# Performance work log

Hardware: AMD Instinct MI355X
Metric: run time of the kernel (lower is better)

Reference implementation:

```python
import jax, jax.numpy as jnp
import numpy as np

N = 8192      # nodes (= hidden_channels / heads)
E = 262144    # edges (avg degree 32)
IN = 256      # in_channels
H = 8         # heads
C = 32        # out_channels per head
NEG_SLOPE = 0.2


def setup_inputs() -> dict:
    key = jax.random.key(0)
    ks = jax.random.split(key, 8)
    x = jax.random.normal(ks[0], (N, IN), jnp.float32)
    edge_index = jax.random.randint(ks[1], (2, E), 0, N, dtype=jnp.int32)
    lin_w = jax.random.normal(ks[2], (H * C, IN), jnp.float32) * (1.0 / np.sqrt(IN))
    att_src = jax.random.normal(ks[3], (H, C), jnp.float32) * 0.1
    att_dst = jax.random.normal(ks[4], (H, C), jnp.float32) * 0.1
    bias = jax.random.normal(ks[5], (H * C,), jnp.float32) * 0.01
    out_w = jax.random.normal(ks[6], (C, N * H * C), jnp.float32) * (1.0 / np.sqrt(N * H * C))
    out_b = jax.random.normal(ks[7], (C,), jnp.float32) * 0.01
    return {"x": x, "edge_index": edge_index, "lin_w": lin_w, "att_src": att_src,
            "att_dst": att_dst, "bias": bias, "out_w": out_w, "out_b": out_b}


def reference(x, edge_index, lin_w, att_src, att_dst, bias, out_w, out_b):
    n = x.shape[0]
    # PyG GATConv default: add self loops
    loop = jnp.arange(n, dtype=edge_index.dtype)
    src = jnp.concatenate([edge_index[0], loop])  # message sources j
    dst = jnp.concatenate([edge_index[1], loop])  # message targets i
    # per-head linear projection: [n, H, C]
    xh = (x @ lin_w.T).reshape(n, H, C)
    a_src = jnp.einsum('nhc,hc->nh', xh, att_src)  # [n, H]
    a_dst = jnp.einsum('nhc,hc->nh', xh, att_dst)  # [n, H]
    # edge attention logits + segment softmax over incoming edges of each dst
    e = jax.nn.leaky_relu(a_src[src] + a_dst[dst], negative_slope=NEG_SLOPE)  # [E', H]
    m = jax.ops.segment_max(e, dst, num_segments=n)        # [n, H]
    ex = jnp.exp(e - m[dst])
    denom = jax.ops.segment_sum(ex, dst, num_segments=n)   # [n, H]
    alpha = ex / denom[dst]                                 # [E', H]
    # weighted scatter-add aggregation
    agg = jax.ops.segment_sum(alpha[:, :, None] * xh[src], dst, num_segments=n)  # [n, H, C]
    out = agg.reshape(n, H * C) + bias
    # flatten all nodes, dense output layer, softmax
    y = out.reshape(-1) @ out_w.T + out_b  # [C]
    return jax.nn.softmax(y)
```

## Files before the change

### kernel.cpp

```cpp
#include <hip/hip_runtime.h>


namespace {
constexpr int  kN    = 8192;
constexpr int  kE    = 262144;
constexpr int  kTotE = kE + kN;
constexpr long kK    = 2097152;
constexpr int  kYB   = 256;
}

typedef float vfloat4 __attribute__((ext_vector_type(4)));

static __device__ __forceinline__ ushort f2bf(float f) {
  unsigned u = __float_as_uint(f);
  return (ushort)((u + 0x7FFFu + ((u >> 16) & 1u)) >> 16);
}
static __device__ __forceinline__ float bf2f(ushort b) {
  return __uint_as_float(((unsigned)b) << 16);
}

__global__ __launch_bounds__(256) void gemm_att_hist(const float* __restrict__ x,
                                                     const float* __restrict__ lw,
                                                     const float* __restrict__ att_s,
                                                     const float* __restrict__ att_d,
                                                     const int* __restrict__ ei,
                                                     ushort* __restrict__ xh_bf,
                                                     float* __restrict__ a_src,
                                                     float* __restrict__ a_dst,
                                                     int* __restrict__ cnt) {
  __shared__ float As[16][68];
  __shared__ float Bs[16][68];
  const int t  = threadIdx.x;
  const int tx = t & 15, ty = t >> 4;
  const int rowBase = blockIdx.x * 64;
  const int colBase = blockIdx.y * 64;
  const int lr = t >> 2;
  const int lk = (t & 3) * 4;

  {
    const int bid = blockIdx.y * 128 + blockIdx.x;
    const int gid = bid * 512 + t;
    atomicAdd(&cnt[ei[kE + gid]], 1);
    atomicAdd(&cnt[ei[kE + gid + 256]], 1);
  }

  float acc[4][4] = {};
  for (int kc = 0; kc < 256; kc += 16) {
    float4 av = *(const float4*)(x  + (long)(rowBase + lr) * 256 + kc + lk);
    float4 bv = *(const float4*)(lw + (long)(colBase + lr) * 256 + kc + lk);
    __syncthreads();
    As[lk + 0][lr] = av.x; As[lk + 1][lr] = av.y; As[lk + 2][lr] = av.z; As[lk + 3][lr] = av.w;
    Bs[lk + 0][lr] = bv.x; Bs[lk + 1][lr] = bv.y; Bs[lk + 2][lr] = bv.z; Bs[lk + 3][lr] = bv.w;
    __syncthreads();
#pragma unroll
    for (int k = 0; k < 16; k++) {
      float4 a4 = *(const float4*)(&As[k][ty * 4]);
      float4 b4 = *(const float4*)(&Bs[k][tx * 4]);
      float aa[4] = {a4.x, a4.y, a4.z, a4.w};
      float bb[4] = {b4.x, b4.y, b4.z, b4.w};
#pragma unroll
      for (int i = 0; i < 4; i++)
#pragma unroll
        for (int j = 0; j < 4; j++) acc[i][j] += aa[i] * bb[j];
    }
  }

#pragma unroll
  for (int i = 0; i < 4; i++) {
    const long row = rowBase + ty * 4 + i;
    ushort4 ob = make_ushort4(f2bf(acc[i][0]), f2bf(acc[i][1]),
                              f2bf(acc[i][2]), f2bf(acc[i][3]));
    *(ushort4*)(xh_bf + row * 256 + colBase + tx * 4) = ob;
  }

  float4 as4 = *(const float4*)(att_s + colBase + tx * 4);
  float4 ad4 = *(const float4*)(att_d + colBase + tx * 4);
#pragma unroll
  for (int i = 0; i < 4; i++) {
    float s = acc[i][0] * as4.x + acc[i][1] * as4.y + acc[i][2] * as4.z + acc[i][3] * as4.w;
    float d = acc[i][0] * ad4.x + acc[i][1] * ad4.y + acc[i][2] * ad4.z + acc[i][3] * ad4.w;
#pragma unroll
    for (int off = 4; off; off >>= 1) {
      s += __shfl_down(s, off, 8);
      d += __shfl_down(d, off, 8);
    }
    if ((tx & 7) == 0) {
      const int row  = rowBase + ty * 4 + i;
      const int head = blockIdx.y * 2 + (tx >> 3);
      a_src[row * 8 + head] = s;
      a_dst[row * 8 + head] = d;
    }
  }
}

__global__ __launch_bounds__(1024) void scan_cnt(const int* __restrict__ cnt,
                                                 int* __restrict__ rowptr,
                                                 int* __restrict__ wpos) {
  __shared__ int wsum[16];
  const int t = threadIdx.x, lane = t & 63, w = t >> 6;
  int v[8]; int sum = 0;
#pragma unroll
  for (int q = 0; q < 8; q++) { v[q] = cnt[t * 8 + q] + 1; sum += v[q]; }
  int sc = sum;
#pragma unroll
  for (int off = 1; off < 64; off <<= 1) {
    int n = __shfl_up(sc, off, 64);
    if (lane >= off) sc += n;
  }
  if (lane == 63) wsum[w] = sc;
  __syncthreads();
  if (t < 16) {
    int ws = wsum[t];
#pragma unroll
    for (int off = 1; off < 16; off <<= 1) {
      int n = __shfl_up(ws, off, 16);
      if ((t & 15) >= off) ws += n;
    }
    wsum[t] = ws;
  }
  __syncthreads();
  int excl = (w ? wsum[w - 1] : 0) + sc - sum;
#pragma unroll
  for (int q = 0; q < 8; q++) {
    rowptr[t * 8 + q] = excl;
    wpos[t * 8 + q]   = excl;
    excl += v[q];
  }
  if (t == 1023) rowptr[kN] = excl;
}

__global__ __launch_bounds__(256) void scatter_csr(const int* __restrict__ ei,
                                                   const float* __restrict__ a_src,
                                                   const float* __restrict__ a_dst,
                                                   int* __restrict__ wpos,
                                                   int* __restrict__ csr,
                                                   float* __restrict__ w8) {
  int idx = blockIdx.x * 256 + threadIdx.x;
  if (idx >= kTotE) return;
  int s, d;
  if (idx < kE) { s = ei[idx]; d = ei[kE + idx]; }
  else          { s = idx - kE; d = s; }
  int pos = atomicAdd(&wpos[d], 1);
  csr[pos] = s;
  float4 s0 = *(const float4*)(a_src + s * 8);
  float4 s1 = *(const float4*)(a_src + s * 8 + 4);
  float4 d0 = *(const float4*)(a_dst + d * 8);
  float4 d1 = *(const float4*)(a_dst + d * 8 + 4);
  float e[8] = {s0.x + d0.x, s0.y + d0.y, s0.z + d0.z, s0.w + d0.w,
                s1.x + d1.x, s1.y + d1.y, s1.z + d1.z, s1.w + d1.w};
  float w[8];
#pragma unroll
  for (int h = 0; h < 8; h++) {
    float ee = (e[h] > 0.f) ? e[h] : 0.2f * e[h];
    w[h] = __expf(ee);
  }
  float4* wp = (float4*)(w8 + (long)pos * 8);
  wp[0] = make_float4(w[0], w[1], w[2], w[3]);
  wp[1] = make_float4(w[4], w[5], w[6], w[7]);
}

__global__ __launch_bounds__(256) void agg_dot(const ushort* __restrict__ xb,
                                               const float* __restrict__ w8,
                                               const int* __restrict__ rowptr,
                                               const int* __restrict__ csr,
                                               const float* __restrict__ bias,
                                               const float* __restrict__ w,
                                               float* __restrict__ ypart) {
  const int i = blockIdx.x, t = threadIdx.x, h = t >> 5;
  const int lane = t & 63, wid = t >> 6;

  const long wbase = (long)i * 256 + lane * 4;
  vfloat4 wv[8];
#pragma unroll
  for (int cc = 0; cc < 8; cc++) {
    const int c = cc * 4 + wid;
    wv[cc] = __builtin_nontemporal_load((const vfloat4*)(w + (long)c * kK + wbase));
  }

  const int beg = rowptr[i], end = rowptr[i + 1];
  float acc = 0.f, den = 0.f;
  int j = beg;
  for (; j + 8 <= end; j += 8) {
    int   s[8]; float ww[8]; float f[8];
#pragma unroll
    for (int q = 0; q < 8; q++) s[q] = csr[j + q];
#pragma unroll
    for (int q = 0; q < 8; q++) ww[q] = w8[(long)(j + q) * 8 + h];
#pragma unroll
    for (int q = 0; q < 8; q++) f[q] = bf2f(xb[(long)s[q] * 256 + t]);
#pragma unroll
    for (int q = 0; q < 8; q++) { den += ww[q]; acc += ww[q] * f[q]; }
  }
  for (; j < end; j++) {
    int s0 = csr[j];
    float w0 = w8[(long)j * 8 + h];
    den += w0;
    acc += w0 * bf2f(xb[(long)s0 * 256 + t]);
  }

  __shared__ float ofs[256];
  __shared__ float yb[32];
  ofs[t] = acc / den + bias[t];
  __syncthreads();
  float4 f4 = *(const float4*)(ofs + lane * 4);
#pragma unroll
  for (int cc = 0; cc < 8; cc++) {
    float p = wv[cc].x * f4.x + wv[cc].y * f4.y + wv[cc].z * f4.z + wv[cc].w * f4.w;
    p += __shfl_down(p, 32, 64);
    p += __shfl_down(p, 16, 64);
    p += __shfl_down(p, 8, 64);
    p += __shfl_down(p, 4, 64);
    p += __shfl_down(p, 2, 64);
    p += __shfl_down(p, 1, 64);
    if (lane == 0) yb[cc * 4 + wid] = p;
  }
  __syncthreads();
  if (t < 32) atomicAdd(&ypart[(i & (kYB - 1)) * 32 + t], yb[t]);
}

__global__ __launch_bounds__(1024) void finalize(const float* __restrict__ ypart,
                                                 const float* __restrict__ ob,
                                                 float* __restrict__ out) {
  __shared__ float s[32][33];
  const int t = threadIdx.x;
  const int c = t & 31, r = t >> 5;
  float sum = 0.f;
  for (int q = r; q < kYB; q += 32) sum += ypart[q * 32 + c];
  s[c][r] = sum;
  __syncthreads();
  if (t < 32) {
    float y = ob[t];
#pragma unroll
    for (int r2 = 0; r2 < 32; r2++) y += s[t][r2];
    float m = y;
#pragma unroll
    for (int off = 16; off; off >>= 1) m = fmaxf(m, __shfl_xor(m, off, 32));
    float e = __expf(y - m);
    float d = e;
#pragma unroll
    for (int off = 16; off; off >>= 1) d += __shfl_xor(d, off, 32);
    out[t] = e / d;
  }
}

extern "C" void kernel_launch(void* const* d_in, const int* in_sizes, int n_in,
                              void* d_out, int out_size, void* d_ws, size_t ws_size,
                              hipStream_t stream) {
  (void)in_sizes; (void)n_in; (void)out_size; (void)ws_size;
  const float* x     = (const float*)d_in[0];
  const int*   ei    = (const int*)  d_in[1];
  const float* lin_w = (const float*)d_in[2];
  const float* att_s = (const float*)d_in[3];
  const float* att_d = (const float*)d_in[4];
  const float* bias  = (const float*)d_in[5];
  const float* out_w = (const float*)d_in[6];
  const float* out_b = (const float*)d_in[7];
  float* out = (float*)d_out;

  float*  a_src    = (float*)d_ws;
  float*  a_dst    = a_src + kN * 8;
  float*  w8       = a_dst + kN * 8;
  ushort* xh_bf    = (ushort*)(w8 + (long)kTotE * 8);
  int*    cnt      = (int*)(xh_bf + kK);
  float*  ypart    = (float*)(cnt + kN);
  int*    rowptr   = (int*)(ypart + kYB * 32);
  int*    wpos     = rowptr + (kN + 1);
  int*    csr      = wpos + kN;

  (void)hipMemsetAsync(cnt, 0, kN * sizeof(int) + kYB * 32 * sizeof(float), stream);
  gemm_att_hist<<<dim3(128, 4), 256, 0, stream>>>(x, lin_w, att_s, att_d, ei,
                                                  xh_bf, a_src, a_dst, cnt);
  scan_cnt   <<<1, 1024, 0, stream>>>(cnt, rowptr, wpos);
  scatter_csr<<<(kTotE + 255) / 256, 256, 0, stream>>>(ei, a_src, a_dst, wpos, csr, w8);
  agg_dot    <<<kN, 256, 0, stream>>>(xh_bf, w8, rowptr, csr, bias, out_w, ypart);
  finalize   <<<1, 1024, 0, stream>>>(ypart, out_b, out);
}
```

Before: 427.0 us.

## Compute edge attention weights inside aggregation instead of materializing w8

Edge weights (leaky-relu plus exp of a_src+a_dst) are no longer computed in the CSR scatter kernel and written to an E'x8 buffer. The aggregation kernel now recomputes them from a_src gathered per source and a_dst per destination. This removes the write and reread of roughly 8.7 MB of per-edge weights and the scatter kernel's extra gathers, at the cost of redundant exp work across the 32 threads per head. The tail loop is folded into the 8-wide loop with masking.

```diff
diff --git a/kernel.cpp b/kernel.cpp
--- a/kernel.cpp
+++ b/kernel.cpp
@@ -130,11 +130,8 @@
 }
 
 __global__ __launch_bounds__(256) void scatter_csr(const int* __restrict__ ei,
-                                                   const float* __restrict__ a_src,
-                                                   const float* __restrict__ a_dst,
                                                    int* __restrict__ wpos,
-                                                   int* __restrict__ csr,
-                                                   float* __restrict__ w8) {
+                                                   int* __restrict__ csr) {
   int idx = blockIdx.x * 256 + threadIdx.x;
   if (idx >= kTotE) return;
   int s, d;
@@ -142,25 +139,11 @@
   else          { s = idx - kE; d = s; }
   int pos = atomicAdd(&wpos[d], 1);
   csr[pos] = s;
-  float4 s0 = *(const float4*)(a_src + s * 8);
-  float4 s1 = *(const float4*)(a_src + s * 8 + 4);
-  float4 d0 = *(const float4*)(a_dst + d * 8);
-  float4 d1 = *(const float4*)(a_dst + d * 8 + 4);
-  float e[8] = {s0.x + d0.x, s0.y + d0.y, s0.z + d0.z, s0.w + d0.w,
-                s1.x + d1.x, s1.y + d1.y, s1.z + d1.z, s1.w + d1.w};
-  float w[8];
-#pragma unroll
-  for (int h = 0; h < 8; h++) {
-    float ee = (e[h] > 0.f) ? e[h] : 0.2f * e[h];
-    w[h] = __expf(ee);
-  }
-  float4* wp = (float4*)(w8 + (long)pos * 8);
-  wp[0] = make_float4(w[0], w[1], w[2], w[3]);
-  wp[1] = make_float4(w[4], w[5], w[6], w[7]);
 }
 
 __global__ __launch_bounds__(256) void agg_dot(const ushort* __restrict__ xb,
-                                               const float* __restrict__ w8,
+                                               const float* __restrict__ a_src,
+                                               const float* __restrict__ a_dst,
                                                const int* __restrict__ rowptr,
                                                const int* __restrict__ csr,
                                                const float* __restrict__ bias,
@@ -169,6 +152,8 @@
   const int i = blockIdx.x, t = threadIdx.x, h = t >> 5;
   const int lane = t & 63, wid = t >> 6;
 
+  const int beg = rowptr[i], end = rowptr[i + 1];
+
   const long wbase = (long)i * 256 + lane * 4;
   vfloat4 wv[8];
 #pragma unroll
@@ -177,25 +162,28 @@
     wv[cc] = __builtin_nontemporal_load((const vfloat4*)(w + (long)c * kK + wbase));
   }
 
-  const int beg = rowptr[i], end = rowptr[i + 1];
+  const float adh = a_dst[i * 8 + h];
+
   float acc = 0.f, den = 0.f;
-  int j = beg;
-  for (; j + 8 <= end; j += 8) {
-    int   s[8]; float ww[8]; float f[8];
-#pragma unroll
-    for (int q = 0; q < 8; q++) s[q] = csr[j + q];
-#pragma unroll
-    for (int q = 0; q < 8; q++) ww[q] = w8[(long)(j + q) * 8 + h];
+  for (int j = beg; j < end; j += 8) {
+    const int lim = end - j;
+    int s[8];
+#pragma unroll
+    for (int q = 0; q < 8; q++) s[q] = csr[(q < lim) ? j + q : j];
+    float as[8];
+#pragma unroll
+    for (int q = 0; q < 8; q++) as[q] = a_src[(long)s[q] * 8 + h];
+    float f[8];
 #pragma unroll
     for (int q = 0; q < 8; q++) f[q] = bf2f(xb[(long)s[q] * 256 + t]);
 #pragma unroll
-    for (int q = 0; q < 8; q++) { den += ww[q]; acc += ww[q] * f[q]; }
-  }
-  for (; j < end; j++) {
-    int s0 = csr[j];
-    float w0 = w8[(long)j * 8 + h];
-    den += w0;
-    acc += w0 * bf2f(xb[(long)s0 * 256 + t]);
+    for (int q = 0; q < 8; q++) {
+      float e  = as[q] + adh;
+      float ee = (e > 0.f) ? e : 0.2f * e;
+      float wq = (q < lim) ? __expf(ee) : 0.f;
+      den += wq;
+      acc += wq * f[q];
+    }
   }
 
   __shared__ float ofs[256];
@@ -259,8 +247,7 @@
 
   float*  a_src    = (float*)d_ws;
   float*  a_dst    = a_src + kN * 8;
-  float*  w8       = a_dst + kN * 8;
-  ushort* xh_bf    = (ushort*)(w8 + (long)kTotE * 8);
+  ushort* xh_bf    = (ushort*)(a_dst + kN * 8);
   int*    cnt      = (int*)(xh_bf + kK);
   float*  ypart    = (float*)(cnt + kN);
   int*    rowptr   = (int*)(ypart + kYB * 32);
@@ -271,7 +258,8 @@
   gemm_att_hist<<<dim3(128, 4), 256, 0, stream>>>(x, lin_w, att_s, att_d, ei,
                                                   xh_bf, a_src, a_dst, cnt);
   scan_cnt   <<<1, 1024, 0, stream>>>(cnt, rowptr, wpos);
-  scatter_csr<<<(kTotE + 255) / 256, 256, 0, stream>>>(ei, a_src, a_dst, wpos, csr, w8);
-  agg_dot    <<<kN, 256, 0, stream>>>(xh_bf, w8, rowptr, csr, bias, out_w, ypart);
+  scatter_csr<<<(kTotE + 255) / 256, 256, 0, stream>>>(ei, wpos, csr);
+  agg_dot    <<<kN, 256, 0, stream>>>(xh_bf, a_src, a_dst, rowptr, csr, bias,
+                                      out_w, ypart);
   finalize   <<<1, 1024, 0, stream>>>(ypart, out_b, out);
 }
```

New measurement: 434.3 us. Within noise of the previous version (+1.7%).
